# Performance work log

Hardware: AMD Instinct MI355X
Metric: run time of the kernel (lower is better)

## Reference

```python
import jax, jax.numpy as jnp
import numpy as np

B, C, H, W = 2, 32, 256, 1216
PT = 6
EPS = 1e-6

def _conv(x, w):
    # 3x3 conv, stride 1, SAME padding, NCHW/OIHW
    return jax.lax.conv_general_dilated(x, w, (1, 1), ((1, 1), (1, 1)),
                                        dimension_numbers=('NCHW', 'OIHW', 'NCHW'))

def _cbn(x, w, s, b):
    # conv (bias=False) + eval-mode BatchNorm folded into per-channel scale/bias
    return _conv(x, w) * s[None, :, None, None] + b[None, :, None, None]

def _cb(x, w, b):
    # conv with bias (no norm branch of Basic2d)
    return _conv(x, w) + b[None, :, None, None]

def _gen_kernel(fout, w1, s1, b1, w2, s2, b2):
    # GenKernel: normalized per-pixel kernel with middle weight = 1 - sum(others)
    h = jax.nn.relu(_cbn(fout, w1, s1, b1))
    w = _cbn(h, w2, s2, b2)  # [B, pk*pk-1, H, W]
    w = w / (jnp.sum(jnp.abs(w), axis=1, keepdims=True) + EPS)
    wmid = 1.0 - jnp.sum(w, axis=1, keepdims=True)
    half = w.shape[1] // 2
    return jnp.concatenate([w[:, :half], wmid, w[:, half:]], axis=1)  # [B, pk*pk, H, W]

def _local_conv(x, w, k):
    # bpconvlocal: per-pixel spatially-varying k x k convolution of a 1-channel map
    p = k // 2
    _, _, Hx, Wx = x.shape
    xp = jnp.pad(x, ((0, 0), (0, 0), (p, p), (p, p)))
    patches = jnp.stack([xp[:, 0, i:i + Hx, j:j + Wx]
                         for i in range(k) for j in range(k)], axis=1)  # [B, k*k, H, W]
    return jnp.sum(w * patches, axis=1, keepdims=True)

def _cspn(fout, hn, h0,
          k3w1, k3s1, k3b1, k3w2, k3s2, k3b2,
          k5w1, k5s1, k5b1, k5w2, k5s2, k5b2,
          k7w1, k7s1, k7b1, k7w2, k7s2, k7b2,
          mw1, ms1, mb1, mw2, mbias2,
          cw1, cs1, cb1, cw2, cbias2,
          tw1, ts1, tb1, tw2, tbias2):
    w3 = _gen_kernel(fout, k3w1, k3s1, k3b1, k3w2, k3s2, k3b2)
    w5 = _gen_kernel(fout, k5w1, k5s1, k5b1, k5w2, k5s2, k5b2)
    w7 = _gen_kernel(fout, k7w1, k7s1, k7b1, k7w2, k7s2, k7b2)
    valid = (h0 > 0.001).astype(fout.dtype)
    mask = jax.nn.sigmoid(_cb(jax.nn.relu(_cbn(fout, mw1, ms1, mb1)), mw2, mbias2)) * valid
    m3, m5, m7 = jnp.split(mask, 3, axis=1)
    conf = jax.nn.softmax(_cb(jax.nn.relu(_cbn(fout, cw1, cs1, cb1)), cw2, cbias2), axis=1)
    c3, c5, c7 = jnp.split(conf, 3, axis=1)
    h3 = h5 = h7 = hn
    hns = [hn]
    for i in range(PT):
        h3 = (1.0 - m3) * _local_conv(h3, w3, 3) + m3 * h0
        h5 = (1.0 - m5) * _local_conv(h5, w5, 5) + m5 * h0
        h7 = (1.0 - m7) * _local_conv(h7, w7, 7) + m7 * h0
        if i == PT // 2 - 1:
            hns.append(c3 * h3 + c5 * h5 + c7 * h7)
    hns.append(c3 * h3 + c5 * h5 + c7 * h7)
    hns = jnp.concatenate(hns, axis=1)  # [B, 3, H, W]
    wt = jax.nn.softmax(_cb(jax.nn.relu(_cbn(jnp.concatenate([fout, hns], axis=1),
                                             tw1, ts1, tb1)), tw2, tbias2), axis=1)
    return jnp.sum(wt * hns, axis=1, keepdims=True)

def setup_inputs():
    key = jax.random.key(0)
    ks = iter(jax.random.split(key, 80))
    def nrm(shape, s=0.05):
        return jax.random.normal(next(ks), shape, dtype=jnp.float32) * s
    d = {}
    d['fout'] = jax.random.normal(next(ks), (B, C, H, W), dtype=jnp.float32)
    d['hn'] = jax.random.uniform(next(ks), (B, 1, H, W), dtype=jnp.float32) * 10.0
    sparse = (jax.random.uniform(next(ks), (B, 1, H, W)) < 0.06).astype(jnp.float32)
    d['h0'] = sparse * jax.random.uniform(next(ks), (B, 1, H, W), dtype=jnp.float32) * 10.0
    for pk, pre in ((3, 'k3'), (5, 'k5'), (7, 'k7')):
        co = pk * pk - 1
        d[pre + 'w1'] = nrm((C, C, 3, 3)); d[pre + 's1'] = 1.0 + nrm((C,)); d[pre + 'b1'] = nrm((C,))
        d[pre + 'w2'] = nrm((co, C, 3, 3)); d[pre + 's2'] = 1.0 + nrm((co,)); d[pre + 'b2'] = nrm((co,))
    for pre, cin in (('m', C), ('c', C), ('t', C + 3)):
        d[pre + 'w1'] = nrm((C, cin, 3, 3)); d[pre + 's1'] = 1.0 + nrm((C,)); d[pre + 'b1'] = nrm((C,))
        d[pre + 'w2'] = nrm((3, C, 3, 3)); d[pre + 'bias2'] = nrm((3,))
    return d

def reference(fout, hn, h0,
              k3w1, k3s1, k3b1, k3w2, k3s2, k3b2,
              k5w1, k5s1, k5b1, k5w2, k5s2, k5b2,
              k7w1, k7s1, k7b1, k7w2, k7s2, k7b2,
              mw1, ms1, mb1, mw2, mbias2,
              cw1, cs1, cb1, cw2, cbias2,
              tw1, ts1, tb1, tw2, tbias2):
    return _cspn(fout, hn, h0,
                 k3w1, k3s1, k3b1, k3w2, k3s2, k3b2,
                 k5w1, k5s1, k5b1, k5w2, k5s2, k5b2,
                 k7w1, k7s1, k7b1, k7w2, k7s2, k7b2,
                 mw1, ms1, mb1, mw2, mbias2,
                 cw1, cs1, cb1, cw2, cbias2,
                 tw1, ts1, tb1, tw2, tbias2)
```

## Files before the change

kernel.cpp:

```cpp
#include <hip/hip_runtime.h>
#include <hip/hip_bf16.h>

constexpr int B_ = 2, H_ = 256, W_ = 1216;
constexpr int HW = H_ * W_;
constexpr int NP = B_ * HW;
constexpr int WP = W_ + 2;
constexpr int HP = H_ + 2;
constexpr int HWP = HP * WP;
constexpr float EPS_ = 1e-6f;

typedef __bf16 bfrag __attribute__((ext_vector_type(8)));
typedef float f4 __attribute__((ext_vector_type(4)));

union BU { uint4 u; bfrag f; };

__device__ __forceinline__ ushort f2b(float x) {
  uint u = __float_as_uint(x);
  u += 0x7fffu + ((u >> 16) & 1u);
  return (ushort)(u >> 16);
}
__device__ __forceinline__ float b2f(ushort u) {
  return __uint_as_float(((uint)u) << 16);
}

__global__ __launch_bounds__(256)
void zring_k(ushort* __restrict__ hP) {
  constexpr int PB = 2 * WP * 4 + 2 * (HP - 2) * 4;
  int i = blockIdx.x * 256 + threadIdx.x;
  if (i >= 2 * PB) return;
  int b = i / PB, r = i % PB;
  size_t idx;
  if (r < WP * 4) idx = (size_t)r;
  else if (r < 2 * WP * 4) idx = (size_t)(HP - 1) * WP * 4 + (r - WP * 4);
  else {
    int q = r - 2 * WP * 4;
    int row = q >> 3, k = q & 7;
    int col = (k < 4) ? k : (WP - 1) * 4 + (k - 4);
    idx = (size_t)(row + 1) * WP * 4 + col;
  }
  *(uint4*)&hP[(size_t)b * HWP * 32 + idx * 8] = uint4{0, 0, 0, 0};
}

__global__ __launch_bounds__(256, 2)
void convs1(const float* __restrict__ xf, const float* __restrict__ wg,
            const float* __restrict__ scale, const float* __restrict__ bias,
            ushort* __restrict__ outh)
{
  __shared__ ushort buf[25344];

  const int tid = threadIdx.x;
  const int lane = tid & 63;
  const int wid = tid >> 6;
  const int x0 = blockIdx.x * 64, y0 = blockIdx.y * 4, b = blockIdx.z;

  for (int i = tid; i < 9 * 32 * 32; i += 256) {
    int ci = i & 31, rest = i >> 5;
    int co = rest & 31, tap = rest >> 5;
    float v = wg[(co * 32 + ci) * 9 + tap];
    ushort hi = f2b(v);
    ushort lo = f2b(v - b2f(hi));
    int idx = (tap * 32 + co) * 32 + ci;
    buf[idx] = hi;
    buf[9216 + idx] = lo;
  }
  __syncthreads();

  bfrag avhi[2][9], avlo[2][9];
#pragma unroll
  for (int tap = 0; tap < 9; ++tap)
#pragma unroll
    for (int mt = 0; mt < 2; ++mt) {
      int idx = ((tap * 32) + mt * 16 + (lane & 15)) * 32 + (lane >> 4) * 8;
      avhi[mt][tap] = *(const bfrag*)&buf[idx];
      avlo[mt][tap] = *(const bfrag*)&buf[9216 + idx];
    }
  __syncthreads();

  for (int i = tid; i < 396 * 4; i += 256) {
    int oct = i & 3, rest = i >> 2;
    int xx = rest % 66, rr = rest / 66;
    int yy = y0 - 1 + rr, x = x0 - 1 + xx;
    uint4 vh = {0, 0, 0, 0}, vl = {0, 0, 0, 0};
    if ((unsigned)yy < (unsigned)H_ && (unsigned)x < (unsigned)W_) {
      const float* src = xf + ((size_t)b * 32 + oct * 8) * HW + (size_t)yy * W_ + x;
      uint uh[4], ul[4];
#pragma unroll
      for (int j = 0; j < 4; ++j) {
        float a = src[(size_t)(2 * j + 0) * HW];
        float c = src[(size_t)(2 * j + 1) * HW];
        ushort ah = f2b(a), ch = f2b(c);
        ushort al = f2b(a - b2f(ah)), cl = f2b(c - b2f(ch));
        uh[j] = (uint)ah | ((uint)ch << 16);
        ul[j] = (uint)al | ((uint)cl << 16);
      }
      vh = uint4{uh[0], uh[1], uh[2], uh[3]};
      vl = uint4{ul[0], ul[1], ul[2], ul[3]};
    }
    *(uint4*)&buf[rest * 32 + oct * 8] = vh;
    *(uint4*)&buf[12672 + rest * 32 + oct * 8] = vl;
  }
  __syncthreads();

  const int n = lane & 15, quad = lane >> 4;

  f4 acc[4][2];
#pragma unroll
  for (int tu = 0; tu < 4; ++tu)
#pragma unroll
    for (int mt = 0; mt < 2; ++mt) acc[tu][mt] = f4{0.f, 0.f, 0.f, 0.f};

#pragma unroll
  for (int tap = 0; tap < 9; ++tap) {
    int dy = tap / 3, dx = tap % 3;
#pragma unroll
    for (int tu = 0; tu < 4; ++tu) {
      int t = wid + tu * 4;
      int r = t >> 2, g = t & 3;
      int pix = (r + dy) * 66 + g * 16 + n + dx;
      bfrag bhi = *(const bfrag*)&buf[pix * 32 + quad * 8];
      bfrag blo = *(const bfrag*)&buf[12672 + pix * 32 + quad * 8];
#pragma unroll
      for (int mt = 0; mt < 2; ++mt) {
        acc[tu][mt] = __builtin_amdgcn_mfma_f32_16x16x32_bf16(avhi[mt][tap], bhi, acc[tu][mt], 0, 0, 0);
        acc[tu][mt] = __builtin_amdgcn_mfma_f32_16x16x32_bf16(avhi[mt][tap], blo, acc[tu][mt], 0, 0, 0);
        acc[tu][mt] = __builtin_amdgcn_mfma_f32_16x16x32_bf16(avlo[mt][tap], bhi, acc[tu][mt], 0, 0, 0);
      }
    }
  }

#pragma unroll
  for (int tu = 0; tu < 4; ++tu) {
    int t = wid + tu * 4;
    int r = t >> 2, g = t & 3;
    int gx = x0 + g * 16 + n, gy = y0 + r;
    size_t bpix = (size_t)b * HWP + (size_t)(gy + 1) * WP + (gx + 1);
#pragma unroll
    for (int mt = 0; mt < 2; ++mt) {
      int cob = mt * 16 + quad * 4;
      float v0 = fmaxf(acc[tu][mt][0] * scale[cob + 0] + bias[cob + 0], 0.f);
      float v1 = fmaxf(acc[tu][mt][1] * scale[cob + 1] + bias[cob + 1], 0.f);
      float v2 = fmaxf(acc[tu][mt][2] * scale[cob + 2] + bias[cob + 2], 0.f);
      float v3 = fmaxf(acc[tu][mt][3] * scale[cob + 3] + bias[cob + 3], 0.f);
      uint u0 = (uint)f2b(v0) | ((uint)f2b(v1) << 16);
      uint u1 = (uint)f2b(v2) | ((uint)f2b(v3) << 16);
      *(uint2*)&outh[bpix * 32 + cob] = uint2{u0, u1};
    }
  }
}

template<int nM, int MINW>
__global__ __launch_bounds__(256, MINW)
void convs2(const ushort* __restrict__ hP, const float* __restrict__ wg,
            const float* __restrict__ scale, const float* __restrict__ bias,
            ushort* __restrict__ outw, int CO)
{
  constexpr int NM16 = nM * 16;
  constexpr int WSZ = 9 * NM16 * 32;
  __shared__ ushort buf[2 * WSZ];

  const int tid = threadIdx.x;
  const int lane = tid & 63;
  const int wid = tid >> 6;
  const int x0 = blockIdx.x * 64, y0 = blockIdx.y * 4, b = blockIdx.z;

  for (int i = tid; i < WSZ; i += 256) {
    int ci = i & 31, rest = i >> 5;
    int co = rest % NM16, tap = rest / NM16;
    float v = (co < CO) ? wg[(co * 32 + ci) * 9 + tap] : 0.f;
    ushort hi = f2b(v);
    ushort lo = f2b(v - b2f(hi));
    buf[i] = lo;
    buf[WSZ + i] = hi;
  }
  __syncthreads();

  bfrag avhi[nM][9];
#pragma unroll
  for (int tap = 0; tap < 9; ++tap)
#pragma unroll
    for (int mt = 0; mt < nM; ++mt)
      avhi[mt][tap] = *(const bfrag*)&buf[WSZ + ((tap * NM16) + mt * 16 + (lane & 15)) * 32 + (lane >> 4) * 8];

  const int n = lane & 15, quad = lane >> 4;
  const ushort* hb = hP + (size_t)b * HWP * 32;

  f4 acc[4][nM];
#pragma unroll
  for (int tu = 0; tu < 4; ++tu)
#pragma unroll
    for (int mt = 0; mt < nM; ++mt) acc[tu][mt] = f4{0.f, 0.f, 0.f, 0.f};

#pragma unroll
  for (int tap = 0; tap < 9; ++tap) {
    int dy = tap / 3, dx = tap % 3;
    bfrag alo[nM];
#pragma unroll
    for (int mt = 0; mt < nM; ++mt)
      alo[mt] = *(const bfrag*)&buf[((tap * NM16) + mt * 16 + (lane & 15)) * 32 + (lane >> 4) * 8];
#pragma unroll
    for (int tu = 0; tu < 4; ++tu) {
      int t = wid + tu * 4;
      int r = t >> 2, g = t & 3;
      int rb = (y0 + r + dy) * WP + x0 + g * 16 + n + dx;
      bfrag bv = *(const bfrag*)&hb[(size_t)rb * 32 + quad * 8];
#pragma unroll
      for (int mt = 0; mt < nM; ++mt) {
        acc[tu][mt] = __builtin_amdgcn_mfma_f32_16x16x32_bf16(avhi[mt][tap], bv, acc[tu][mt], 0, 0, 0);
        acc[tu][mt] = __builtin_amdgcn_mfma_f32_16x16x32_bf16(alo[mt], bv, acc[tu][mt], 0, 0, 0);
      }
    }
  }

#pragma unroll
  for (int tu = 0; tu < 4; ++tu) {
    int t = wid + tu * 4;
    int r = t >> 2, g = t & 3;
    int gx = x0 + g * 16 + n, gy = y0 + r;
    size_t gpix = (size_t)gy * W_ + gx;

    float vs[nM][4];
    float pa = 0.f;
#pragma unroll
    for (int mt = 0; mt < nM; ++mt)
#pragma unroll
      for (int rg = 0; rg < 4; ++rg) {
        int co = mt * 16 + quad * 4 + rg;
        float v = (co < CO) ? acc[tu][mt][rg] * scale[co] + bias[co] : 0.f;
        vs[mt][rg] = v;
        pa += fabsf(v);
      }
    pa += __shfl_xor(pa, 16);
    pa += __shfl_xor(pa, 32);
    float inv = 1.f / (pa + EPS_);
#pragma unroll
    for (int mt = 0; mt < nM; ++mt)
#pragma unroll
      for (int rg = 0; rg < 4; ++rg) {
        int co = mt * 16 + quad * 4 + rg;
        if (co < CO)
          outw[((size_t)b * CO + co) * HW + gpix] = f2b(vs[mt][rg] * inv);
      }
  }
}

template<int KB2, int MINW>
__global__ __launch_bounds__(256, MINW)
void conv1p(const float* __restrict__ xf, const float* __restrict__ hnsp,
            const float* __restrict__ wg, const float* __restrict__ scale,
            const float* __restrict__ bias, ushort* __restrict__ outh)
{
  constexpr int CIN = KB2 ? 35 : 32;
  __shared__ ushort wl[9 * 32 * 32];
  __shared__ ushort xl[396 * 32];
  __shared__ ushort wl2[KB2 ? 9 * 32 * 8 : 8];
  __shared__ ushort xl2[KB2 ? 396 * 8 : 8];

  const int tid = threadIdx.x;
  const int lane = tid & 63;
  const int wid = tid >> 6;
  const int x0 = blockIdx.x * 64, y0 = blockIdx.y * 4, b = blockIdx.z;

  for (int i = tid; i < 9 * 32 * 32; i += 256) {
    int ci = i & 31, rest = i >> 5;
    int co = rest & 31, tap = rest >> 5;
    float v = wg[(co * CIN + ci) * 9 + tap];
    wl[(tap * 32 + co) * 32 + ci] = f2b(v);
  }
  if (KB2) {
    for (int i = tid; i < 9 * 32 * 8; i += 256) {
      int c8 = i & 7, rest = i >> 3;
      int co = rest & 31, tap = rest >> 5;
      int cc = (c8 < 3) ? c8 : ((c8 < 6) ? c8 - 3 : -1);
      float v = (cc >= 0) ? wg[(co * 35 + 32 + cc) * 9 + tap] : 0.f;
      wl2[(tap * 32 + co) * 8 + c8] = f2b(v);
    }
    for (int i = tid; i < 396; i += 256) {
      int xx = i % 66, rr = i / 66;
      int yy = y0 - 1 + rr, x = x0 - 1 + xx;
      float v0 = 0.f, v1 = 0.f, v2 = 0.f;
      if ((unsigned)yy < (unsigned)H_ && (unsigned)x < (unsigned)W_) {
        size_t pix = (size_t)yy * W_ + x;
        v0 = hnsp[((size_t)b * 3 + 0) * HW + pix];
        v1 = hnsp[((size_t)b * 3 + 1) * HW + pix];
        v2 = hnsp[((size_t)b * 3 + 2) * HW + pix];
      }
      ushort h0b = f2b(v0), h1b = f2b(v1), h2b = f2b(v2);
      ushort l0 = f2b(v0 - b2f(h0b)), l1 = f2b(v1 - b2f(h1b)), l2 = f2b(v2 - b2f(h2b));
      uint u0 = (uint)h0b | ((uint)h1b << 16);
      uint u1 = (uint)h2b | ((uint)l0 << 16);
      uint u2 = (uint)l1 | ((uint)l2 << 16);
      *(uint4*)&xl2[i * 8] = uint4{u0, u1, u2, 0};
    }
  }
  for (int i = tid; i < 396 * 4; i += 256) {
    int oct = i & 3, rest = i >> 2;
    int xx = rest % 66, rr = rest / 66;
    int yy = y0 - 1 + rr, x = x0 - 1 + xx;
    uint4 v = {0, 0, 0, 0};
    if ((unsigned)yy < (unsigned)H_ && (unsigned)x < (unsigned)W_) {
      const float* src = xf + ((size_t)b * 32 + oct * 8) * HW + (size_t)yy * W_ + x;
      uint u[4];
#pragma unroll
      for (int j = 0; j < 4; ++j) {
        float a = src[(size_t)(2 * j + 0) * HW];
        float c = src[(size_t)(2 * j + 1) * HW];
        u[j] = (uint)f2b(a) | ((uint)f2b(c) << 16);
      }
      v = uint4{u[0], u[1], u[2], u[3]};
    }
    *(uint4*)&xl[rest * 32 + oct * 8] = v;
  }
  __syncthreads();

  bfrag av[2][9];
#pragma unroll
  for (int tap = 0; tap < 9; ++tap)
#pragma unroll
    for (int mt = 0; mt < 2; ++mt)
      av[mt][tap] = *(const bfrag*)&wl[((tap * 32) + mt * 16 + (lane & 15)) * 32 + (lane >> 4) * 8];
  bfrag a2[KB2 ? 2 : 1][KB2 ? 9 : 1];
  if (KB2) {
#pragma unroll
    for (int tap = 0; tap < 9; ++tap)
#pragma unroll
      for (int mt = 0; mt < 2; ++mt) {
        BU t; t.u = uint4{0, 0, 0, 0};
        if (lane < 16) t.f = *(const bfrag*)&wl2[(tap * 32 + mt * 16 + lane) * 8];
        a2[mt][tap] = t.f;
      }
  }

  const int n = lane & 15, quad = lane >> 4;

  f4 acc[4][2];
#pragma unroll
  for (int tu = 0; tu < 4; ++tu)
#pragma unroll
    for (int mt = 0; mt < 2; ++mt) acc[tu][mt] = f4{0.f, 0.f, 0.f, 0.f};

#pragma unroll
  for (int tap = 0; tap < 9; ++tap) {
    int dy = tap / 3, dx = tap % 3;
#pragma unroll
    for (int tu = 0; tu < 4; ++tu) {
      int t = wid + tu * 4;
      int r = t >> 2, g = t & 3;
      int pix = (r + dy) * 66 + g * 16 + n + dx;
      bfrag bv = *(const bfrag*)&xl[pix * 32 + quad * 8];
#pragma unroll
      for (int mt = 0; mt < 2; ++mt)
        acc[tu][mt] = __builtin_amdgcn_mfma_f32_16x16x32_bf16(av[mt][tap], bv, acc[tu][mt], 0, 0, 0);
      if (KB2) {
        BU t2; t2.u = uint4{0, 0, 0, 0};
        if (lane < 16) t2.f = *(const bfrag*)&xl2[pix * 8];
#pragma unroll
        for (int mt = 0; mt < 2; ++mt)
          acc[tu][mt] = __builtin_amdgcn_mfma_f32_16x16x32_bf16(a2[mt][tap], t2.f, acc[tu][mt], 0, 0, 0);
      }
    }
  }

#pragma unroll
  for (int tu = 0; tu < 4; ++tu) {
    int t = wid + tu * 4;
    int r = t >> 2, g = t & 3;
    int gx = x0 + g * 16 + n, gy = y0 + r;
    size_t bpix = (size_t)b * HWP + (size_t)(gy + 1) * WP + (gx + 1);
#pragma unroll
    for (int mt = 0; mt < 2; ++mt) {
      int cob = mt * 16 + quad * 4;
      float v0 = fmaxf(acc[tu][mt][0] * scale[cob + 0] + bias[cob + 0], 0.f);
      float v1 = fmaxf(acc[tu][mt][1] * scale[cob + 1] + bias[cob + 1], 0.f);
      float v2 = fmaxf(acc[tu][mt][2] * scale[cob + 2] + bias[cob + 2], 0.f);
      float v3 = fmaxf(acc[tu][mt][3] * scale[cob + 3] + bias[cob + 3], 0.f);
      uint u0 = (uint)f2b(v0) | ((uint)f2b(v1) << 16);
      uint u1 = (uint)f2b(v2) | ((uint)f2b(v3) << 16);
      *(uint2*)&outh[bpix * 32 + cob] = uint2{u0, u1};
    }
  }
}

template<int EPI>
__global__ __launch_bounds__(256, 4)
void conv2g(const ushort* __restrict__ hP, const float* __restrict__ wg,
            const float* __restrict__ bias, const float* __restrict__ h0,
            const float* __restrict__ hnsp, float* __restrict__ outf)
{
  __shared__ ushort wl[9 * 16 * 32];

  const int tid = threadIdx.x;
  const int lane = tid & 63;
  const int wid = tid >> 6;
  const int x0 = blockIdx.x * 64, y0 = blockIdx.y * 4, b = blockIdx.z;

  for (int i = tid; i < 9 * 16 * 32; i += 256) {
    int ci = i & 31, rest = i >> 5;
    int co = rest & 15, tap = rest >> 4;
    float v = (co < 3) ? wg[(co * 32 + ci) * 9 + tap] : 0.f;
    wl[(tap * 16 + co) * 32 + ci] = f2b(v);
  }
  __syncthreads();

  bfrag av[9];
#pragma unroll
  for (int tap = 0; tap < 9; ++tap)
    av[tap] = *(const bfrag*)&wl[((tap * 16) + (lane & 15)) * 32 + (lane >> 4) * 8];

  const int n = lane & 15, quad = lane >> 4;
  const ushort* hb = hP + (size_t)b * HWP * 32;

  f4 acc[4];
#pragma unroll
  for (int tu = 0; tu < 4; ++tu) acc[tu] = f4{0.f, 0.f, 0.f, 0.f};

#pragma unroll
  for (int tap = 0; tap < 9; ++tap) {
    int dy = tap / 3, dx = tap % 3;
#pragma unroll
    for (int tu = 0; tu < 4; ++tu) {
      int t = wid + tu * 4;
      int r = t >> 2, g = t & 3;
      int rb = (y0 + r + dy) * WP + x0 + g * 16 + n + dx;
      bfrag bv = *(const bfrag*)&hb[(size_t)rb * 32 + quad * 8];
      acc[tu] = __builtin_amdgcn_mfma_f32_16x16x32_bf16(av[tap], bv, acc[tu], 0, 0, 0);
    }
  }

#pragma unroll
  for (int tu = 0; tu < 4; ++tu) {
    int t = wid + tu * 4;
    int r = t >> 2, g = t & 3;
    int gx = x0 + g * 16 + n, gy = y0 + r;
    size_t gpix = (size_t)gy * W_ + gx;
    size_t bpix = (size_t)b * HW + gpix;

    if constexpr (EPI == 2) {
      if (lane < 16) {
        float valid = (h0[bpix] > 0.001f) ? 1.f : 0.f;
#pragma unroll
        for (int rg = 0; rg < 3; ++rg) {
          float v = acc[tu][rg] + bias[rg];
          float sg = 1.f / (1.f + expf(-v));
          outf[((size_t)b * 3 + rg) * HW + gpix] = sg * valid;
        }
      }
    } else if constexpr (EPI == 3) {
      if (lane < 16) {
        float v0 = acc[tu][0] + bias[0];
        float v1 = acc[tu][1] + bias[1];
        float v2 = acc[tu][2] + bias[2];
        float m = fmaxf(v0, fmaxf(v1, v2));
        float e0 = expf(v0 - m), e1 = expf(v1 - m), e2 = expf(v2 - m);
        float inv = 1.f / (e0 + e1 + e2);
        outf[((size_t)b * 3 + 0) * HW + gpix] = e0 * inv;
        outf[((size_t)b * 3 + 1) * HW + gpix] = e1 * inv;
        outf[((size_t)b * 3 + 2) * HW + gpix] = e2 * inv;
      }
    } else if constexpr (EPI == 4) {
      if (lane < 16) {
        float v0 = acc[tu][0] + bias[0];
        float v1 = acc[tu][1] + bias[1];
        float v2 = acc[tu][2] + bias[2];
        float m = fmaxf(v0, fmaxf(v1, v2));
        float e0 = expf(v0 - m), e1 = expf(v1 - m), e2 = expf(v2 - m);
        float inv = 1.f / (e0 + e1 + e2);
        float a0 = hnsp[((size_t)b * 3 + 0) * HW + gpix];
        float a1 = hnsp[((size_t)b * 3 + 1) * HW + gpix];
        float a2v = hnsp[((size_t)b * 3 + 2) * HW + gpix];
        outf[bpix] = (e0 * a0 + e1 * a1 + e2 * a2v) * inv;
      }
    }
  }
}

__global__ __launch_bounds__(256)
void init_k(const float* __restrict__ hn, float* __restrict__ h3,
            float* __restrict__ h5, float* __restrict__ h7,
            float* __restrict__ hns)
{
  int t = blockIdx.x * 256 + threadIdx.x;
  if (t >= NP) return;
  float v = hn[t];
  h3[t] = v; h5[t] = v; h7[t] = v;
  int b = t / HW, rem = t - b * HW;
  hns[(size_t)b * 3 * HW + rem] = v;
}

__global__ __launch_bounds__(256)
void iterate_k(const float* __restrict__ h3i, const float* __restrict__ h5i,
               const float* __restrict__ h7i,
               float* __restrict__ h3o, float* __restrict__ h5o,
               float* __restrict__ h7o,
               const ushort* __restrict__ w3, const ushort* __restrict__ w5,
               const ushort* __restrict__ w7,
               const float* __restrict__ mask, const float* __restrict__ h0,
               float* __restrict__ hns, int chn, const float* __restrict__ conf)
{
  int t = blockIdx.x * 256 + threadIdx.x;
  if (t >= NP) return;
  int b = t / HW;
  int rem = t - b * HW;
  int y = rem / W_;
  int x = rem - y * W_;
  size_t pb = (size_t)b * HW;

  float h0v = h0[t];

  float s3 = 0.f, ws3 = 0.f;
#pragma unroll
  for (int p = 0; p < 8; ++p) {
    int tap = (p < 4) ? p : p + 1;
    int dy = tap / 3 - 1, dx = tap % 3 - 1;
    int yy = y + dy, xx = x + dx;
    float hv = ((unsigned)yy < (unsigned)H_ && (unsigned)xx < (unsigned)W_)
                   ? h3i[pb + yy * W_ + xx] : 0.f;
    float wv = b2f(w3[(size_t)(b * 8 + p) * HW + rem]);
    ws3 += wv;
    s3 += wv * hv;
  }
  s3 += (1.f - ws3) * h3i[t];
  float m3 = mask[(size_t)(b * 3 + 0) * HW + rem];
  float n3 = (1.f - m3) * s3 + m3 * h0v;
  h3o[t] = n3;

  float s5 = 0.f, ws5 = 0.f;
#pragma unroll
  for (int p = 0; p < 24; ++p) {
    int tap = (p < 12) ? p : p + 1;
    int dy = tap / 5 - 2, dx = tap % 5 - 2;
    int yy = y + dy, xx = x + dx;
    float hv = ((unsigned)yy < (unsigned)H_ && (unsigned)xx < (unsigned)W_)
                   ? h5i[pb + yy * W_ + xx] : 0.f;
    float wv = b2f(w5[(size_t)(b * 24 + p) * HW + rem]);
    ws5 += wv;
    s5 += wv * hv;
  }
  s5 += (1.f - ws5) * h5i[t];
  float m5 = mask[(size_t)(b * 3 + 1) * HW + rem];
  float n5 = (1.f - m5) * s5 + m5 * h0v;
  h5o[t] = n5;

  float s7 = 0.f, ws7 = 0.f;
#pragma unroll
  for (int p = 0; p < 48; ++p) {
    int tap = (p < 24) ? p : p + 1;
    int dy = tap / 7 - 3, dx = tap % 7 - 3;
    int yy = y + dy, xx = x + dx;
    float hv = ((unsigned)yy < (unsigned)H_ && (unsigned)xx < (unsigned)W_)
                   ? h7i[pb + yy * W_ + xx] : 0.f;
    float wv = b2f(w7[(size_t)(b * 48 + p) * HW + rem]);
    ws7 += wv;
    s7 += wv * hv;
  }
  s7 += (1.f - ws7) * h7i[t];
  float m7 = mask[(size_t)(b * 3 + 2) * HW + rem];
  float n7 = (1.f - m7) * s7 + m7 * h0v;
  h7o[t] = n7;

  if (chn >= 0) {
    float c3 = conf[(size_t)(b * 3 + 0) * HW + rem];
    float c5 = conf[(size_t)(b * 3 + 1) * HW + rem];
    float c7 = conf[(size_t)(b * 3 + 2) * HW + rem];
    hns[(size_t)(b * 3 + chn) * HW + rem] = c3 * n3 + c5 * n5 + c7 * n7;
  }
}

extern "C" void kernel_launch(void* const* d_in, const int* in_sizes, int n_in,
                              void* d_out, int out_size, void* d_ws, size_t ws_size,
                              hipStream_t stream) {
  const float* fout = (const float*)d_in[0];
  const float* hn   = (const float*)d_in[1];
  const float* h0   = (const float*)d_in[2];
  const float* k3w1 = (const float*)d_in[3];
  const float* k3s1 = (const float*)d_in[4];
  const float* k3b1 = (const float*)d_in[5];
  const float* k3w2 = (const float*)d_in[6];
  const float* k3s2 = (const float*)d_in[7];
  const float* k3b2 = (const float*)d_in[8];
  const float* k5w1 = (const float*)d_in[9];
  const float* k5s1 = (const float*)d_in[10];
  const float* k5b1 = (const float*)d_in[11];
  const float* k5w2 = (const float*)d_in[12];
  const float* k5s2 = (const float*)d_in[13];
  const float* k5b2 = (const float*)d_in[14];
  const float* k7w1 = (const float*)d_in[15];
  const float* k7s1 = (const float*)d_in[16];
  const float* k7b1 = (const float*)d_in[17];
  const float* k7w2 = (const float*)d_in[18];
  const float* k7s2 = (const float*)d_in[19];
  const float* k7b2 = (const float*)d_in[20];
  const float* mw1  = (const float*)d_in[21];
  const float* ms1  = (const float*)d_in[22];
  const float* mb1  = (const float*)d_in[23];
  const float* mw2  = (const float*)d_in[24];
  const float* mbias2 = (const float*)d_in[25];
  const float* cw1  = (const float*)d_in[26];
  const float* cs1  = (const float*)d_in[27];
  const float* cb1  = (const float*)d_in[28];
  const float* cw2  = (const float*)d_in[29];
  const float* cbias2 = (const float*)d_in[30];
  const float* tw1  = (const float*)d_in[31];
  const float* ts1  = (const float*)d_in[32];
  const float* tb1  = (const float*)d_in[33];
  const float* tw2  = (const float*)d_in[34];
  const float* tbias2 = (const float*)d_in[35];

  float* out = (float*)d_out;

  size_t hP_elems = (size_t)2 * HWP * 32;
  size_t need = hP_elems * 2 + (size_t)NP * (80 * 2 + 15 * 4);
  if (ws_size < need) return;
  ushort* hPb  = (ushort*)d_ws;
  ushort* w3   = hPb  + hP_elems;
  ushort* w5   = w3   + (size_t)8 * NP;
  ushort* w7   = w5   + (size_t)24 * NP;
  float* mask  = (float*)(w7 + (size_t)48 * NP);
  float* conf  = mask + (size_t)3 * NP;
  float* hA    = conf + (size_t)3 * NP;
  float* hns   = hA   + (size_t)6 * NP;

  dim3 blk(256);
  dim3 gc(W_ / 64, H_ / 4, B_);
  int ge = NP / 256;
  constexpr int PB = 2 * WP * 4 + 2 * (HP - 2) * 4;
  int gz = (2 * PB + 255) / 256;

  zring_k<<<gz, blk, 0, stream>>>(hPb);

  convs1<<<gc, blk, 0, stream>>>(fout, k3w1, k3s1, k3b1, hPb);
  convs2<1, 4><<<gc, blk, 0, stream>>>(hPb, k3w2, k3s2, k3b2, w3, 8);
  convs1<<<gc, blk, 0, stream>>>(fout, k5w1, k5s1, k5b1, hPb);
  convs2<2, 2><<<gc, blk, 0, stream>>>(hPb, k5w2, k5s2, k5b2, w5, 24);
  convs1<<<gc, blk, 0, stream>>>(fout, k7w1, k7s1, k7b1, hPb);
  convs2<3, 2><<<gc, blk, 0, stream>>>(hPb, k7w2, k7s2, k7b2, w7, 48);

  conv1p<0, 3><<<gc, blk, 0, stream>>>(fout, nullptr, mw1, ms1, mb1, hPb);
  conv2g<2><<<gc, blk, 0, stream>>>(hPb, mw2, mbias2, h0, nullptr, mask);

  conv1p<0, 3><<<gc, blk, 0, stream>>>(fout, nullptr, cw1, cs1, cb1, hPb);
  conv2g<3><<<gc, blk, 0, stream>>>(hPb, cw2, cbias2, nullptr, nullptr, conf);

  float* h3c = hA + (size_t)0 * NP; float* h3n = hA + (size_t)1 * NP;
  float* h5c = hA + (size_t)2 * NP; float* h5n = hA + (size_t)3 * NP;
  float* h7c = hA + (size_t)4 * NP; float* h7n = hA + (size_t)5 * NP;

  init_k<<<ge, blk, 0, stream>>>(hn, h3c, h5c, h7c, hns);
  for (int i = 0; i < 6; ++i) {
    int chn = (i == 2) ? 1 : ((i == 5) ? 2 : -1);
    iterate_k<<<ge, blk, 0, stream>>>(h3c, h5c, h7c, h3n, h5n, h7n,
                                      w3, w5, w7, mask, h0, hns, chn, conf);
    float* t;
    t = h3c; h3c = h3n; h3n = t;
    t = h5c; h5c = h5n; h5n = t;
    t = h7c; h7c = h7n; h7n = t;
  }

  conv1p<1, 2><<<gc, blk, 0, stream>>>(fout, hns, tw1, ts1, tb1, hPb);
  conv2g<4><<<gc, blk, 0, stream>>>(hPb, tw2, tbias2, nullptr, hns, out);
}
```

Measured before the change: 1.041 ms.

## Pre-pack conv weights to bf16 once and load from global instead of per-block LDS

A new prep kernel converts all conv weights into bf16 hi/lo split layouts once per call, stored in workspace. Every conv kernel now loads its weight fragments per tap straight from this global buffer, instead of converting fp32 weights into LDS in every block. This removes redundant per-block conversion, LDS traffic and syncs, and cuts register and LDS pressure. The launch-bounds occupancy targets are raised to match. The trade-off is per-tap global (cache-resident) weight loads inside the MFMA loop and one extra kernel launch.

```diff
diff --git a/kernel.cpp b/kernel.cpp
--- a/kernel.cpp
+++ b/kernel.cpp
@@ -9,6 +9,21 @@
 constexpr int HWP = HP * WP;
 constexpr float EPS_ = 1e-6f;
 
+constexpr int PW1_K3 = 0;
+constexpr int PW1_K5 = 18432;
+constexpr int PW1_K7 = 36864;
+constexpr int PW2_K3 = 55296;
+constexpr int PW2_K5 = 64512;
+constexpr int PW2_K7 = 82944;
+constexpr int PP1_M  = 110592;
+constexpr int PP1_C  = 119808;
+constexpr int PP1_T  = 129024;
+constexpr int PP1T2  = 138240;
+constexpr int PG2_M  = 140544;
+constexpr int PG2_C  = 145152;
+constexpr int PG2_T  = 149760;
+constexpr int PREP_N = 154368;
+
 typedef __bf16 bfrag __attribute__((ext_vector_type(8)));
 typedef float f4 __attribute__((ext_vector_type(4)));
 
@@ -21,6 +36,66 @@
 }
 __device__ __forceinline__ float b2f(ushort u) {
   return __uint_as_float(((uint)u) << 16);
+}
+
+__global__ __launch_bounds__(256)
+void prep_k(const float* __restrict__ k3w1, const float* __restrict__ k5w1,
+            const float* __restrict__ k7w1, const float* __restrict__ k3w2,
+            const float* __restrict__ k5w2, const float* __restrict__ k7w2,
+            const float* __restrict__ mw1, const float* __restrict__ cw1,
+            const float* __restrict__ tw1, const float* __restrict__ mw2,
+            const float* __restrict__ cw2, const float* __restrict__ tw2,
+            ushort* __restrict__ wp)
+{
+  int i = blockIdx.x * 256 + threadIdx.x;
+  if (i >= PREP_N) return;
+  ushort outv;
+  if (i < PW2_K3) {
+    int c = i / 18432, r = i % 18432;
+    const float* src = (c == 0) ? k3w1 : (c == 1) ? k5w1 : k7w1;
+    int ci = r & 31; int t1 = r >> 5;
+    int co = t1 & 31; int t2 = t1 >> 5;
+    int tap = t2 % 9, half = t2 / 9;
+    float v = src[(co * 32 + ci) * 9 + tap];
+    ushort hi = f2b(v);
+    outv = half ? f2b(v - b2f(hi)) : hi;
+  } else if (i < PP1_M) {
+    int r = i - PW2_K3;
+    const float* src; int NM16, CO;
+    if (r < 9216)       { src = k3w2; NM16 = 16; CO = 8; }
+    else if (r < 27648) { src = k5w2; NM16 = 32; CO = 24; r -= 9216; }
+    else                { src = k7w2; NM16 = 48; CO = 48; r -= 27648; }
+    int ci = r & 31; int t1 = r >> 5;
+    int co = t1 % NM16; int t2 = t1 / NM16;
+    int tap = t2 % 9, half = t2 / 9;
+    if (co < CO) {
+      float v = src[(co * 32 + ci) * 9 + tap];
+      ushort hi = f2b(v);
+      outv = half ? f2b(v - b2f(hi)) : hi;
+    } else outv = 0;
+  } else if (i < PP1T2) {
+    int r = i - PP1_M;
+    int c = r / 9216; r %= 9216;
+    const float* src = (c == 0) ? mw1 : (c == 1) ? cw1 : tw1;
+    int CIN = (c == 2) ? 35 : 32;
+    int ci = r & 31; int t1 = r >> 5;
+    int co = t1 & 31, tap = t1 >> 5;
+    outv = f2b(src[(co * CIN + ci) * 9 + tap]);
+  } else if (i < PG2_M) {
+    int r = i - PP1T2;
+    int c8 = r & 7; int t1 = r >> 3;
+    int co = t1 & 31, tap = t1 >> 5;
+    int cc = (c8 < 3) ? c8 : ((c8 < 6) ? c8 - 3 : -1);
+    outv = (cc >= 0) ? f2b(tw1[(co * 35 + 32 + cc) * 9 + tap]) : (ushort)0;
+  } else {
+    int r = i - PG2_M;
+    int c = r / 4608; r %= 4608;
+    const float* src = (c == 0) ? mw2 : (c == 1) ? cw2 : tw2;
+    int ci = r & 31; int t1 = r >> 5;
+    int co = t1 & 15, tap = t1 >> 4;
+    outv = (co < 3) ? f2b(src[(co * 32 + ci) * 9 + tap]) : (ushort)0;
+  }
+  wp[i] = outv;
 }
 
 __global__ __launch_bounds__(256)
@@ -41,40 +116,17 @@
   *(uint4*)&hP[(size_t)b * HWP * 32 + idx * 8] = uint4{0, 0, 0, 0};
 }
 
-__global__ __launch_bounds__(256, 2)
-void convs1(const float* __restrict__ xf, const float* __restrict__ wg,
+__global__ __launch_bounds__(256, 3)
+void convs1(const float* __restrict__ xf, const ushort* __restrict__ wp,
             const float* __restrict__ scale, const float* __restrict__ bias,
             ushort* __restrict__ outh)
 {
-  __shared__ ushort buf[25344];
+  __shared__ ushort xl[25344];
 
   const int tid = threadIdx.x;
   const int lane = tid & 63;
   const int wid = tid >> 6;
   const int x0 = blockIdx.x * 64, y0 = blockIdx.y * 4, b = blockIdx.z;
-
-  for (int i = tid; i < 9 * 32 * 32; i += 256) {
-    int ci = i & 31, rest = i >> 5;
-    int co = rest & 31, tap = rest >> 5;
-    float v = wg[(co * 32 + ci) * 9 + tap];
-    ushort hi = f2b(v);
-    ushort lo = f2b(v - b2f(hi));
-    int idx = (tap * 32 + co) * 32 + ci;
-    buf[idx] = hi;
-    buf[9216 + idx] = lo;
-  }
-  __syncthreads();
-
-  bfrag avhi[2][9], avlo[2][9];
-#pragma unroll
-  for (int tap = 0; tap < 9; ++tap)
-#pragma unroll
-    for (int mt = 0; mt < 2; ++mt) {
-      int idx = ((tap * 32) + mt * 16 + (lane & 15)) * 32 + (lane >> 4) * 8;
-      avhi[mt][tap] = *(const bfrag*)&buf[idx];
-      avlo[mt][tap] = *(const bfrag*)&buf[9216 + idx];
-    }
-  __syncthreads();
 
   for (int i = tid; i < 396 * 4; i += 256) {
     int oct = i & 3, rest = i >> 2;
@@ -96,8 +148,8 @@
       vh = uint4{uh[0], uh[1], uh[2], uh[3]};
       vl = uint4{ul[0], ul[1], ul[2], ul[3]};
     }
-    *(uint4*)&buf[rest * 32 + oct * 8] = vh;
-    *(uint4*)&buf[12672 + rest * 32 + oct * 8] = vl;
+    *(uint4*)&xl[rest * 32 + oct * 8] = vh;
+    *(uint4*)&xl[12672 + rest * 32 + oct * 8] = vl;
   }
   __syncthreads();
 
@@ -112,18 +164,24 @@
 #pragma unroll
   for (int tap = 0; tap < 9; ++tap) {
     int dy = tap / 3, dx = tap % 3;
+    bfrag avhi[2], avlo[2];
+#pragma unroll
+    for (int mt = 0; mt < 2; ++mt) {
+      avhi[mt] = *(const bfrag*)&wp[((tap * 32) + mt * 16 + n) * 32 + quad * 8];
+      avlo[mt] = *(const bfrag*)&wp[(((9 + tap) * 32) + mt * 16 + n) * 32 + quad * 8];
+    }
 #pragma unroll
     for (int tu = 0; tu < 4; ++tu) {
       int t = wid + tu * 4;
       int r = t >> 2, g = t & 3;
       int pix = (r + dy) * 66 + g * 16 + n + dx;
-      bfrag bhi = *(const bfrag*)&buf[pix * 32 + quad * 8];
-      bfrag blo = *(const bfrag*)&buf[12672 + pix * 32 + quad * 8];
+      bfrag bhi = *(const bfrag*)&xl[pix * 32 + quad * 8];
+      bfrag blo = *(const bfrag*)&xl[12672 + pix * 32 + quad * 8];
 #pragma unroll
       for (int mt = 0; mt < 2; ++mt) {
-        acc[tu][mt] = __builtin_amdgcn_mfma_f32_16x16x32_bf16(avhi[mt][tap], bhi, acc[tu][mt], 0, 0, 0);
-        acc[tu][mt] = __builtin_amdgcn_mfma_f32_16x16x32_bf16(avhi[mt][tap], blo, acc[tu][mt], 0, 0, 0);
-        acc[tu][mt] = __builtin_amdgcn_mfma_f32_16x16x32_bf16(avlo[mt][tap], bhi, acc[tu][mt], 0, 0, 0);
+        acc[tu][mt] = __builtin_amdgcn_mfma_f32_16x16x32_bf16(avhi[mt], bhi, acc[tu][mt], 0, 0, 0);
+        acc[tu][mt] = __builtin_amdgcn_mfma_f32_16x16x32_bf16(avhi[mt], blo, acc[tu][mt], 0, 0, 0);
+        acc[tu][mt] = __builtin_amdgcn_mfma_f32_16x16x32_bf16(avlo[mt], bhi, acc[tu][mt], 0, 0, 0);
       }
     }
   }
@@ -150,37 +208,16 @@
 
 template<int nM, int MINW>
 __global__ __launch_bounds__(256, MINW)
-void convs2(const ushort* __restrict__ hP, const float* __restrict__ wg,
+void convs2(const ushort* __restrict__ hP, const ushort* __restrict__ wp,
             const float* __restrict__ scale, const float* __restrict__ bias,
             ushort* __restrict__ outw, int CO)
 {
   constexpr int NM16 = nM * 16;
-  constexpr int WSZ = 9 * NM16 * 32;
-  __shared__ ushort buf[2 * WSZ];
-
   const int tid = threadIdx.x;
   const int lane = tid & 63;
   const int wid = tid >> 6;
   const int x0 = blockIdx.x * 64, y0 = blockIdx.y * 4, b = blockIdx.z;
 
-  for (int i = tid; i < WSZ; i += 256) {
-    int ci = i & 31, rest = i >> 5;
-    int co = rest % NM16, tap = rest / NM16;
-    float v = (co < CO) ? wg[(co * 32 + ci) * 9 + tap] : 0.f;
-    ushort hi = f2b(v);
-    ushort lo = f2b(v - b2f(hi));
-    buf[i] = lo;
-    buf[WSZ + i] = hi;
-  }
-  __syncthreads();
-
-  bfrag avhi[nM][9];
-#pragma unroll
-  for (int tap = 0; tap < 9; ++tap)
-#pragma unroll
-    for (int mt = 0; mt < nM; ++mt)
-      avhi[mt][tap] = *(const bfrag*)&buf[WSZ + ((tap * NM16) + mt * 16 + (lane & 15)) * 32 + (lane >> 4) * 8];
-
   const int n = lane & 15, quad = lane >> 4;
   const ushort* hb = hP + (size_t)b * HWP * 32;
 
@@ -193,10 +230,12 @@
 #pragma unroll
   for (int tap = 0; tap < 9; ++tap) {
     int dy = tap / 3, dx = tap % 3;
-    bfrag alo[nM];
-#pragma unroll
-    for (int mt = 0; mt < nM; ++mt)
-      alo[mt] = *(const bfrag*)&buf[((tap * NM16) + mt * 16 + (lane & 15)) * 32 + (lane >> 4) * 8];
+    bfrag whi[nM], wlo[nM];
+#pragma unroll
+    for (int mt = 0; mt < nM; ++mt) {
+      whi[mt] = *(const bfrag*)&wp[((tap * NM16) + mt * 16 + n) * 32 + quad * 8];
+      wlo[mt] = *(const bfrag*)&wp[((9 * NM16) + tap * NM16 + mt * 16 + n) * 32 + quad * 8];
+    }
 #pragma unroll
     for (int tu = 0; tu < 4; ++tu) {
       int t = wid + tu * 4;
@@ -205,8 +244,8 @@
       bfrag bv = *(const bfrag*)&hb[(size_t)rb * 32 + quad * 8];
 #pragma unroll
       for (int mt = 0; mt < nM; ++mt) {
-        acc[tu][mt] = __builtin_amdgcn_mfma_f32_16x16x32_bf16(avhi[mt][tap], bv, acc[tu][mt], 0, 0, 0);
-        acc[tu][mt] = __builtin_amdgcn_mfma_f32_16x16x32_bf16(alo[mt], bv, acc[tu][mt], 0, 0, 0);
+        acc[tu][mt] = __builtin_amdgcn_mfma_f32_16x16x32_bf16(whi[mt], bv, acc[tu][mt], 0, 0, 0);
+        acc[tu][mt] = __builtin_amdgcn_mfma_f32_16x16x32_bf16(wlo[mt], bv, acc[tu][mt], 0, 0, 0);
       }
     }
   }
@@ -246,13 +285,11 @@
 template<int KB2, int MINW>
 __global__ __launch_bounds__(256, MINW)
 void conv1p(const float* __restrict__ xf, const float* __restrict__ hnsp,
-            const float* __restrict__ wg, const float* __restrict__ scale,
-            const float* __restrict__ bias, ushort* __restrict__ outh)
+            const ushort* __restrict__ wp, const ushort* __restrict__ wp2,
+            const float* __restrict__ scale, const float* __restrict__ bias,
+            ushort* __restrict__ outh)
 {
-  constexpr int CIN = KB2 ? 35 : 32;
-  __shared__ ushort wl[9 * 32 * 32];
   __shared__ ushort xl[396 * 32];
-  __shared__ ushort wl2[KB2 ? 9 * 32 * 8 : 8];
   __shared__ ushort xl2[KB2 ? 396 * 8 : 8];
 
   const int tid = threadIdx.x;
@@ -260,20 +297,7 @@
   const int wid = tid >> 6;
   const int x0 = blockIdx.x * 64, y0 = blockIdx.y * 4, b = blockIdx.z;
 
-  for (int i = tid; i < 9 * 32 * 32; i += 256) {
-    int ci = i & 31, rest = i >> 5;
-    int co = rest & 31, tap = rest >> 5;
-    float v = wg[(co * CIN + ci) * 9 + tap];
-    wl[(tap * 32 + co) * 32 + ci] = f2b(v);
-  }
   if (KB2) {
-    for (int i = tid; i < 9 * 32 * 8; i += 256) {
-      int c8 = i & 7, rest = i >> 3;
-      int co = rest & 31, tap = rest >> 5;
-      int cc = (c8 < 3) ? c8 : ((c8 < 6) ? c8 - 3 : -1);
-      float v = (cc >= 0) ? wg[(co * 35 + 32 + cc) * 9 + tap] : 0.f;
-      wl2[(tap * 32 + co) * 8 + c8] = f2b(v);
-    }
     for (int i = tid; i < 396; i += 256) {
       int xx = i % 66, rr = i / 66;
       int yy = y0 - 1 + rr, x = x0 - 1 + xx;
@@ -312,35 +336,30 @@
   }
   __syncthreads();
 
-  bfrag av[2][9];
-#pragma unroll
-  for (int tap = 0; tap < 9; ++tap)
+  const int n = lane & 15, quad = lane >> 4;
+
+  f4 acc[4][2];
+#pragma unroll
+  for (int tu = 0; tu < 4; ++tu)
+#pragma unroll
+    for (int mt = 0; mt < 2; ++mt) acc[tu][mt] = f4{0.f, 0.f, 0.f, 0.f};
+
+#pragma unroll
+  for (int tap = 0; tap < 9; ++tap) {
+    int dy = tap / 3, dx = tap % 3;
+    bfrag av[2];
 #pragma unroll
     for (int mt = 0; mt < 2; ++mt)
-      av[mt][tap] = *(const bfrag*)&wl[((tap * 32) + mt * 16 + (lane & 15)) * 32 + (lane >> 4) * 8];
-  bfrag a2[KB2 ? 2 : 1][KB2 ? 9 : 1];
-  if (KB2) {
-#pragma unroll
-    for (int tap = 0; tap < 9; ++tap)
+      av[mt] = *(const bfrag*)&wp[((tap * 32) + mt * 16 + n) * 32 + quad * 8];
+    bfrag a2[KB2 ? 2 : 1];
+    if (KB2) {
 #pragma unroll
       for (int mt = 0; mt < 2; ++mt) {
         BU t; t.u = uint4{0, 0, 0, 0};
-        if (lane < 16) t.f = *(const bfrag*)&wl2[(tap * 32 + mt * 16 + lane) * 8];
-        a2[mt][tap] = t.f;
-      }
-  }
-
-  const int n = lane & 15, quad = lane >> 4;
-
-  f4 acc[4][2];
-#pragma unroll
-  for (int tu = 0; tu < 4; ++tu)
-#pragma unroll
-    for (int mt = 0; mt < 2; ++mt) acc[tu][mt] = f4{0.f, 0.f, 0.f, 0.f};
-
-#pragma unroll
-  for (int tap = 0; tap < 9; ++tap) {
-    int dy = tap / 3, dx = tap % 3;
+        if (lane < 16) t.f = *(const bfrag*)&wp2[(tap * 32 + mt * 16 + lane) * 8];
+        a2[mt] = t.f;
+      }
+    }
 #pragma unroll
     for (int tu = 0; tu < 4; ++tu) {
       int t = wid + tu * 4;
@@ -349,13 +368,13 @@
       bfrag bv = *(const bfrag*)&xl[pix * 32 + quad * 8];
 #pragma unroll
       for (int mt = 0; mt < 2; ++mt)
-        acc[tu][mt] = __builtin_amdgcn_mfma_f32_16x16x32_bf16(av[mt][tap], bv, acc[tu][mt], 0, 0, 0);
+        acc[tu][mt] = __builtin_amdgcn_mfma_f32_16x16x32_bf16(av[mt], bv, acc[tu][mt], 0, 0, 0);
       if (KB2) {
         BU t2; t2.u = uint4{0, 0, 0, 0};
         if (lane < 16) t2.f = *(const bfrag*)&xl2[pix * 8];
 #pragma unroll
         for (int mt = 0; mt < 2; ++mt)
-          acc[tu][mt] = __builtin_amdgcn_mfma_f32_16x16x32_bf16(a2[mt][tap], t2.f, acc[tu][mt], 0, 0, 0);
+          acc[tu][mt] = __builtin_amdgcn_mfma_f32_16x16x32_bf16(a2[mt], t2.f, acc[tu][mt], 0, 0, 0);
       }
     }
   }
@@ -382,31 +401,21 @@
 
 template<int EPI>
 __global__ __launch_bounds__(256, 4)
-void conv2g(const ushort* __restrict__ hP, const float* __restrict__ wg,
+void conv2g(const ushort* __restrict__ hP, const ushort* __restrict__ wp,
             const float* __restrict__ bias, const float* __restrict__ h0,
             const float* __restrict__ hnsp, float* __restrict__ outf)
 {
-  __shared__ ushort wl[9 * 16 * 32];
-
   const int tid = threadIdx.x;
   const int lane = tid & 63;
   const int wid = tid >> 6;
   const int x0 = blockIdx.x * 64, y0 = blockIdx.y * 4, b = blockIdx.z;
-
-  for (int i = tid; i < 9 * 16 * 32; i += 256) {
-    int ci = i & 31, rest = i >> 5;
-    int co = rest & 15, tap = rest >> 4;
-    float v = (co < 3) ? wg[(co * 32 + ci) * 9 + tap] : 0.f;
-    wl[(tap * 16 + co) * 32 + ci] = f2b(v);
-  }
-  __syncthreads();
+  const int n = lane & 15, quad = lane >> 4;
 
   bfrag av[9];
 #pragma unroll
   for (int tap = 0; tap < 9; ++tap)
-    av[tap] = *(const bfrag*)&wl[((tap * 16) + (lane & 15)) * 32 + (lane >> 4) * 8];
-
-  const int n = lane & 15, quad = lane >> 4;
+    av[tap] = *(const bfrag*)&wp[((tap * 16) + n) * 32 + quad * 8];
+
   const ushort* hb = hP + (size_t)b * HWP * 32;
 
   f4 acc[4];
@@ -608,7 +617,7 @@
   float* out = (float*)d_out;
 
   size_t hP_elems = (size_t)2 * HWP * 32;
-  size_t need = hP_elems * 2 + (size_t)NP * (80 * 2 + 15 * 4);
+  size_t need = hP_elems * 2 + (size_t)NP * (80 * 2 + 15 * 4) + (size_t)PREP_N * 2;
   if (ws_size < need) return;
   ushort* hPb  = (ushort*)d_ws;
   ushort* w3   = hPb  + hP_elems;
@@ -618,27 +627,31 @@
   float* conf  = mask + (size_t)3 * NP;
   float* hA    = conf + (size_t)3 * NP;
   float* hns   = hA   + (size_t)6 * NP;
+  ushort* wp   = (ushort*)(hns + (size_t)3 * NP);
 
   dim3 blk(256);
   dim3 gc(W_ / 64, H_ / 4, B_);
   int ge = NP / 256;
   constexpr int PB = 2 * WP * 4 + 2 * (HP - 2) * 4;
   int gz = (2 * PB + 255) / 256;
-
+  int gp = (PREP_N + 255) / 256;
+
+  prep_k<<<gp, blk, 0, stream>>>(k3w1, k5w1, k7w1, k3w2, k5w2, k7w2,
+                                 mw1, cw1, tw1, mw2, cw2, tw2, wp);
   zring_k<<<gz, blk, 0, stream>>>(hPb);
 
-  convs1<<<gc, blk, 0, stream>>>(fout, k3w1, k3s1, k3b1, hPb);
-  convs2<1, 4><<<gc, blk, 0, stream>>>(hPb, k3w2, k3s2, k3b2, w3, 8);
-  convs1<<<gc, blk, 0, stream>>>(fout, k5w1, k5s1, k5b1, hPb);
-  convs2<2, 2><<<gc, blk, 0, stream>>>(hPb, k5w2, k5s2, k5b2, w5, 24);
-  convs1<<<gc, blk, 0, stream>>>(fout, k7w1, k7s1, k7b1, hPb);
-  convs2<3, 2><<<gc, blk, 0, stream>>>(hPb, k7w2, k7s2, k7b2, w7, 48);
-
-  conv1p<0, 3><<<gc, blk, 0, stream>>>(fout, nullptr, mw1, ms1, mb1, hPb);
-  conv2g<2><<<gc, blk, 0, stream>>>(hPb, mw2, mbias2, h0, nullptr, mask);
-
-  conv1p<0, 3><<<gc, blk, 0, stream>>>(fout, nullptr, cw1, cs1, cb1, hPb);
-  conv2g<3><<<gc, blk, 0, stream>>>(hPb, cw2, cbias2, nullptr, nullptr, conf);
+  convs1<<<gc, blk, 0, stream>>>(fout, wp + PW1_K3, k3s1, k3b1, hPb);
+  convs2<1, 4><<<gc, blk, 0, stream>>>(hPb, wp + PW2_K3, k3s2, k3b2, w3, 8);
+  convs1<<<gc, blk, 0, stream>>>(fout, wp + PW1_K5, k5s1, k5b1, hPb);
+  convs2<2, 4><<<gc, blk, 0, stream>>>(hPb, wp + PW2_K5, k5s2, k5b2, w5, 24);
+  convs1<<<gc, blk, 0, stream>>>(fout, wp + PW1_K7, k7s1, k7b1, hPb);
+  convs2<3, 3><<<gc, blk, 0, stream>>>(hPb, wp + PW2_K7, k7s2, k7b2, w7, 48);
+
+  conv1p<0, 4><<<gc, blk, 0, stream>>>(fout, nullptr, wp + PP1_M, nullptr, ms1, mb1, hPb);
+  conv2g<2><<<gc, blk, 0, stream>>>(hPb, wp + PG2_M, mbias2, h0, nullptr, mask);
+
+  conv1p<0, 4><<<gc, blk, 0, stream>>>(fout, nullptr, wp + PP1_C, nullptr, cs1, cb1, hPb);
+  conv2g<3><<<gc, blk, 0, stream>>>(hPb, wp + PG2_C, cbias2, nullptr, nullptr, conf);
 
   float* h3c = hA + (size_t)0 * NP; float* h3n = hA + (size_t)1 * NP;
   float* h5c = hA + (size_t)2 * NP; float* h5n = hA + (size_t)3 * NP;
@@ -655,6 +668,6 @@
     t = h7c; h7c = h7n; h7n = t;
   }
 
-  conv1p<1, 2><<<gc, blk, 0, stream>>>(fout, hns, tw1, ts1, tb1, hPb);
-  conv2g<4><<<gc, blk, 0, stream>>>(hPb, tw2, tbias2, nullptr, hns, out);
-}
+  conv1p<1, 3><<<gc, blk, 0, stream>>>(fout, hns, wp + PP1_T, wp + PP1T2, ts1, tb1, hPb);
+  conv2g<4><<<gc, blk, 0, stream>>>(hPb, wp + PG2_T, tbias2, nullptr, hns, out);
+}
```

Result: faster. 910.7 us (-12.5%).
